# Kernel optimization log

Hardware: AMD Instinct MI355X
Metric: run time of the kernel (lower is better)

The kernel has to match this reference:

```python
import jax, jax.numpy as jnp
import numpy as np
from functools import partial

K = 3
P = K * K * K          # 27 kernel points
G = 2                  # groups
PAD = 1
STRIDE = 1
DIL = 1
AXIS_SCALE = (0.5, 1.0, 1.0)   # (x, y, z) offset axis scale
CUR_SCALE = 0.5                # warmup scale at global_step=0
EPS = 1e-5


def setup_inputs() -> dict:
    key = jax.random.key(0)
    ks = jax.random.split(key, 8)
    C, OC = 64, 64
    N, D, H, W = 1, 32, 32, 32
    inp = {
        "x": jax.random.normal(ks[0], (N, C, D, H, W), jnp.float32),
        "dw_w": jax.random.normal(ks[1], (C, 1, K, K, K), jnp.float32) * 0.1,
        "gn_w": jnp.ones((C,), jnp.float32),
        "gn_b": jnp.zeros((C,), jnp.float32),
        "inp_w": jax.random.normal(ks[2], (C, C), jnp.float32) * (1.0 / np.sqrt(C)),
        "inp_b": jnp.zeros((C,), jnp.float32),
        # offset/mask weights are zero-init in the module; use small random values
        # so the deformable sampling path is exercised nontrivially.
        "off_w": jax.random.normal(ks[3], (C, G * P * 3), jnp.float32) * 0.01,
        "off_b": jnp.zeros((G * P * 3,), jnp.float32),
        "mask_w": jax.random.normal(ks[4], (C, G * P), jnp.float32) * 0.01,
        "mask_b": jnp.tile(jnp.full((P,), -5.0, jnp.float32).at[P // 2].set(0.0), (G,)),
        "out_w": jax.random.normal(ks[5], (C, OC), jnp.float32) * (1.0 / np.sqrt(C)),
        "out_b": jnp.zeros((OC,), jnp.float32),
    }
    return inp


def _trilinear(vol, loc):
    # vol: [Dp, Hp, Wp, gc]; loc: [..., 3] with (x, y, z) in [-1, 1]
    # grid_sample semantics: align_corners=False, padding_mode='zeros'
    Dp, Hp, Wp, _ = vol.shape
    ix = (loc[..., 0] + 1.0) * 0.5 * Wp - 0.5
    iy = (loc[..., 1] + 1.0) * 0.5 * Hp - 0.5
    iz = (loc[..., 2] + 1.0) * 0.5 * Dp - 0.5
    x0f, y0f, z0f = jnp.floor(ix), jnp.floor(iy), jnp.floor(iz)
    fx, fy, fz = ix - x0f, iy - y0f, iz - z0f
    x0, y0, z0 = x0f.astype(jnp.int32), y0f.astype(jnp.int32), z0f.astype(jnp.int32)
    out = jnp.zeros(loc.shape[:-1] + (vol.shape[-1],), vol.dtype)
    for dz in (0, 1):
        wz = fz if dz else 1.0 - fz
        cz = z0 + dz
        for dy in (0, 1):
            wy = fy if dy else 1.0 - fy
            cy = y0 + dy
            for dx in (0, 1):
                wx = fx if dx else 1.0 - fx
                cx = x0 + dx
                valid = ((cz >= 0) & (cz < Dp) & (cy >= 0) & (cy < Hp)
                         & (cx >= 0) & (cx < Wp))
                v = vol[jnp.clip(cz, 0, Dp - 1),
                        jnp.clip(cy, 0, Hp - 1),
                        jnp.clip(cx, 0, Wp - 1)]  # [..., gc]
                out = out + (wz * wy * wx * valid.astype(vol.dtype))[..., None] * v
    return out


def _forward(x, dw_w, gn_w, gn_b, inp_w, inp_b, off_w, off_b,
             mask_w, mask_b, out_w, out_b):
    N, C, D, H, W = x.shape
    gc = C // G
    # --- dw_conv: depthwise conv3d + GroupNorm(1, C) + GELU ---
    xc = jax.lax.conv_general_dilated(
        x, dw_w, window_strides=(1, 1, 1), padding=[(PAD, PAD)] * 3,
        dimension_numbers=("NCDHW", "OIDHW", "NCDHW"), feature_group_count=C)
    mu = xc.mean(axis=(1, 2, 3, 4), keepdims=True)
    var = ((xc - mu) ** 2).mean(axis=(1, 2, 3, 4), keepdims=True)
    xn = (xc - mu) * jax.lax.rsqrt(var + EPS)
    xn = xn * gn_w[None, :, None, None, None] + gn_b[None, :, None, None, None]
    x1 = jnp.transpose(jax.nn.gelu(xn), (0, 2, 3, 4, 1))       # [N,D,H,W,C]
    # --- offset / mask / input projection ---
    offset = x1 @ off_w + off_b                                  # [N,D,H,W,G*P*3]
    mask = jax.nn.softmax(
        (x1 @ mask_w + mask_b).reshape(N, D, H, W, G, P), axis=-1)
    xp = jnp.transpose(x, (0, 2, 3, 4, 1)) @ inp_w + inp_b       # [N,D,H,W,C]
    # --- core deformable sampling ---
    x_pad = jnp.pad(xp, ((0, 0), (PAD, PAD), (PAD, PAD), (PAD, PAD), (0, 0)))
    Dp, Hp, Wp = D + 2 * PAD, H + 2 * PAD, W + 2 * PAD
    Do = (D + 2 * PAD - DIL * (K - 1) - 1) // STRIDE + 1
    Ho = (H + 2 * PAD - DIL * (K - 1) - 1) // STRIDE + 1
    Wo = (W + 2 * PAD - DIL * (K - 1) - 1) // STRIDE + 1
    # reference grid (x/Wp, y/Hp, z/Dp)
    zc, yc, xc_ = jnp.meshgrid(jnp.arange(Do, dtype=jnp.float32),
                               jnp.arange(Ho, dtype=jnp.float32),
                               jnp.arange(Wo, dtype=jnp.float32), indexing="ij")
    ref = jnp.stack(((xc_ * STRIDE + PAD + 0.5) / Wp,
                     (yc * STRIDE + PAD + 0.5) / Hp,
                     (zc * STRIDE + PAD + 0.5) / Dp), axis=-1)   # [Do,Ho,Wo,3]
    # kernel grid
    lin = jnp.linspace(-(K - 1) // 2, (K - 1) // 2, K, dtype=jnp.float32)
    kz, ky, kx = jnp.meshgrid(lin, lin, lin, indexing="ij")
    kgrid = jnp.stack((kx * DIL / Wp, ky * DIL / Hp, kz * DIL / Dp),
                      axis=-1).reshape(P, 3)
    off = offset.reshape(N, Do, Ho, Wo, G, P, 3)
    off_norm = off / jnp.array([Wp, Hp, Dp], jnp.float32)
    axis = jnp.array(AXIS_SCALE, jnp.float32)
    loc = (ref[None, :, :, :, None, None, :]
           + kgrid[None, None, None, None, None, :, :]
           + off_norm * axis * CUR_SCALE)
    loc = loc * 2.0 - 1.0                                        # [N,Do,Ho,Wo,G,P,3]
    vol = jnp.transpose(x_pad.reshape(N, Dp, Hp, Wp, G, gc),
                        (0, 4, 1, 2, 3, 5))                      # [N,G,Dp,Hp,Wp,gc]
    locs = jnp.transpose(loc, (0, 4, 1, 2, 3, 5, 6))             # [N,G,Do,Ho,Wo,P,3]
    sampled = jax.vmap(jax.vmap(_trilinear))(vol, locs)          # [N,G,Do,Ho,Wo,P,gc]
    out = jnp.einsum("ngdhwpc,ndhwgp->ndhwgc", sampled, mask)
    out = out.reshape(N, Do, Ho, Wo, C)
    return out @ out_w + out_b                                   # [N,Do,Ho,Wo,OC]


def reference(x, dw_w, gn_w, gn_b, inp_w, inp_b, off_w, off_b,
              mask_w, mask_b, out_w, out_b):
    return _forward(x, dw_w, gn_w, gn_b, inp_w, inp_b, off_w, off_b,
                    mask_w, mask_b, out_w, out_b)
```

## Files before the change

kernel.cpp:

```cpp
#include <hip/hip_runtime.h>
#include <hip/hip_fp16.h>
#include <math.h>

#define SP 32768
#define PW 38
#define PW2 (PW*PW)
#define PVOX (PW*PW*PW)
#define OMS 228

typedef short bf16x8 __attribute__((ext_vector_type(8)));
typedef unsigned short u16x4 __attribute__((ext_vector_type(4)));
typedef float f32x4 __attribute__((ext_vector_type(4)));

__device__ __forceinline__ unsigned short f2b(float f) {
    unsigned u = __float_as_uint(f);
    u = (u + 0x7FFFu + ((u >> 16) & 1u)) >> 16;
    return (unsigned short)u;
}
__device__ __forceinline__ float b2f1(unsigned short s) {
    return __uint_as_float(((unsigned)s) << 16);
}
__device__ __forceinline__ __half2 h2(unsigned u) {
    return *reinterpret_cast<__half2*>(&u);
}
__device__ __forceinline__ int vox_of(int sb, int v) {
    int tw = sb & 7, th = (sb >> 3) & 15, td = sb >> 7;
    int vw = v & 3, vh = (v >> 2) & 1, vd = v >> 3;
    return (((td << 1) + vd) << 10) + (((th << 1) + vh) << 5) + (tw << 2) + vw;
}

__global__ void k_front(const float* __restrict__ x, const float* __restrict__ dw,
                        const float* __restrict__ off_w, const float* __restrict__ mask_w,
                        const float* __restrict__ off_b, const float* __restrict__ mask_b,
                        const float* __restrict__ inp_w, const float* __restrict__ out_w,
                        unsigned short* __restrict__ WcatB, float* __restrict__ bcat,
                        unsigned short* __restrict__ inpB, unsigned short* __restrict__ outB,
                        unsigned short* __restrict__ x_tb,
                        unsigned short* __restrict__ xcb, float* __restrict__ partials,
                        unsigned short* __restrict__ xpad) {
    int bb = blockIdx.x, tid = threadIdx.x;
    if (bb < 88) {
        int idx = bb * 256 + tid;
        int j = idx >> 6, k = idx & 63;
        if (j < 224) {
            float v = 0.f;
            if (j < 162) v = off_w[k * 162 + j];
            else if (j < 216) v = mask_w[k * 54 + (j - 162)];
            WcatB[j * 64 + k] = f2b(v);
            if (k == 0) bcat[j] = (j < 162) ? off_b[j] : (j < 216 ? mask_b[j - 162] : 0.f);
        } else if (j < 288) {
            outB[(j - 224) * 64 + k] = f2b(out_w[k * 64 + (j - 224)]);
        } else {
            inpB[(j - 288) * 64 + k] = f2b(inp_w[k * 64 + (j - 288)]);
        }
        return;
    }
    if (bb < 600) {
        __shared__ unsigned short tile[64][66];
        int s0 = (bb - 88) * 64;
        int row = tid >> 6, lane = tid & 63;
        for (int c = row; c < 64; c += 4)
            tile[c][lane] = f2b(x[(size_t)c * SP + s0 + lane]);
        __syncthreads();
        for (int r = row; r < 64; r += 4)
            x_tb[(size_t)(s0 + r) * 64 + lane] = tile[lane][r];
        return;
    }
    if (bb < 2648) {
        int b4 = bb - 600;
        int e4 = b4 * 256 + tid;
        int c = e4 >> 13, s4 = (e4 & 8191) << 2;
        int d = s4 >> 10, h = (s4 >> 5) & 31, w0 = s4 & 31;
        const float* xs = x + (size_t)c * SP;
        const float* wt = dw + c * 27;
        float a0 = 0.f, a1 = 0.f, a2 = 0.f, a3 = 0.f;
#pragma unroll
        for (int kd = 0; kd < 3; ++kd) {
            int zz = d + kd - 1; if ((unsigned)zz >= 32u) continue;
#pragma unroll
            for (int kh = 0; kh < 3; ++kh) {
                int yy = h + kh - 1; if ((unsigned)yy >= 32u) continue;
                const float* row = xs + (zz << 10) + (yy << 5) + w0;
                float4 L = *(const float4*)row;
                float xl = (w0 > 0) ? row[-1] : 0.f;
                float xr = (w0 < 28) ? row[4] : 0.f;
                const float* wr = wt + kd * 9 + kh * 3;
                float wm = wr[0], wc = wr[1], wp = wr[2];
                a0 = __builtin_fmaf(wm, xl,  __builtin_fmaf(wc, L.x, __builtin_fmaf(wp, L.y, a0)));
                a1 = __builtin_fmaf(wm, L.x, __builtin_fmaf(wc, L.y, __builtin_fmaf(wp, L.z, a1)));
                a2 = __builtin_fmaf(wm, L.y, __builtin_fmaf(wc, L.z, __builtin_fmaf(wp, L.w, a2)));
                a3 = __builtin_fmaf(wm, L.z, __builtin_fmaf(wc, L.w, __builtin_fmaf(wp, xr,  a3)));
            }
        }
        u16x4 o4; o4[0] = f2b(a0); o4[1] = f2b(a1); o4[2] = f2b(a2); o4[3] = f2b(a3);
        *(u16x4*)(xcb + (size_t)e4 * 4) = o4;
        __shared__ float rs[256], rq[256];
        rs[tid] = a0 + a1 + a2 + a3;
        rq[tid] = a0 * a0 + a1 * a1 + a2 * a2 + a3 * a3;
        __syncthreads();
        for (int off = 128; off > 0; off >>= 1) {
            if (tid < off) { rs[tid] += rs[tid + off]; rq[tid] += rq[tid + off]; }
            __syncthreads();
        }
        if (tid == 0) {
            partials[b4 * 2 + 0] = rs[0];
            partials[b4 * 2 + 1] = rq[0];
        }
        return;
    }
    int cblk = bb - 2648;
    int j = tid >> 4, c4 = tid & 15;
    u16x4 z = {0, 0, 0, 0};
#pragma unroll
    for (int k = 0; k < 4; ++k) {
        int v = cblk * 64 + k * 16 + j;
        if (v >= PVOX) break;
        int zz = v / PW2, r = v - zz * PW2, yy = r / PW, xx = r - yy * PW;
        if (zz < 2 || zz > 33 || yy < 2 || yy > 33 || xx < 2 || xx > 33)
            *(u16x4*)(xpad + (size_t)v * 64 + c4 * 4) = z;
    }
}

__global__ void k_mid(const unsigned short* __restrict__ xcb, const float* __restrict__ partials,
                      const float* __restrict__ gn_w, const float* __restrict__ gn_b,
                      unsigned short* __restrict__ x1b,
                      const unsigned short* __restrict__ x_tb,
                      const unsigned short* __restrict__ inpB,
                      const float* __restrict__ inp_b,
                      unsigned short* __restrict__ xpad) {
    int bb = blockIdx.x, tid = threadIdx.x;
    if (bb < 512) {
        __shared__ float rs[256], rq[256];
        __shared__ unsigned short tile[64][66];
        float a = 0.f, b = 0.f;
        for (int i = tid; i < 2048; i += 256) { a += partials[2 * i]; b += partials[2 * i + 1]; }
        rs[tid] = a; rq[tid] = b;
        __syncthreads();
        for (int off = 128; off > 0; off >>= 1) {
            if (tid < off) { rs[tid] += rs[tid + off]; rq[tid] += rq[tid + off]; }
            __syncthreads();
        }
        const float Minv = 1.f / 2097152.f;
        float mu = rs[0] * Minv;
        float var = rq[0] * Minv - mu * mu;
        float rsq = rsqrtf(var + 1e-5f);
        int s0 = bb * 64;
        int row = tid >> 6, lane = tid & 63;
        for (int c = row; c < 64; c += 4) {
            float v = (b2f1(xcb[(size_t)c * SP + s0 + lane]) - mu) * rsq * gn_w[c] + gn_b[c];
            float t2 = 1.5957691216057308f * (v + 0.044715f * v * v * v);
            tile[c][lane] = f2b(v / (1.f + __expf(-t2)));
        }
        __syncthreads();
        for (int r = row; r < 64; r += 4)
            x1b[(size_t)(s0 + r) * 64 + lane] = tile[lane][r];
        return;
    }
    {
        int wv = tid >> 6, lane = tid & 63;
        int quad = lane >> 4, col = lane & 15;
        int s0 = (bb - 512) * 64 + wv * 16;
        bf16x8 a0 = *(const bf16x8*)(x_tb + (size_t)(s0 + col) * 64 + quad * 8);
        bf16x8 a1 = *(const bf16x8*)(x_tb + (size_t)(s0 + col) * 64 + 32 + quad * 8);
        int vp[4];
#pragma unroll
        for (int r = 0; r < 4; ++r) {
            int s = s0 + (quad << 2) + r;
            vp[r] = (((s >> 10) + 2) * PW + ((s >> 5) & 31) + 2) * PW + (s & 31) + 2;
        }
#pragma unroll
        for (int nt = 0; nt < 4; ++nt) {
            int n0 = nt * 16;
            bf16x8 b0 = *(const bf16x8*)(inpB + (n0 + col) * 64 + quad * 8);
            bf16x8 b1 = *(const bf16x8*)(inpB + (n0 + col) * 64 + 32 + quad * 8);
            f32x4 c = {0.f, 0.f, 0.f, 0.f};
            c = __builtin_amdgcn_mfma_f32_16x16x32_bf16(a0, b0, c, 0, 0, 0);
            c = __builtin_amdgcn_mfma_f32_16x16x32_bf16(a1, b1, c, 0, 0, 0);
            float bq = inp_b[n0 + col];
#pragma unroll
            for (int r = 0; r < 4; ++r)
                xpad[(size_t)vp[r] * 64 + n0 + col] =
                    __half_as_ushort(__float2half(c[r] + bq));
        }
    }
}

template<int P0, int NP>
__device__ __forceinline__ void sampleN(const float* __restrict__ orow,
                                        const float* __restrict__ mrow,
                                        const char* __restrict__ volc,
                                        float xb, float yb, float zb,
                                        float* __restrict__ acc) {
#pragma unroll
    for (int i = 0; i < NP; ++i) {
        const int p = P0 + i;
        const int px = p % 3, py = (p / 3) % 3, pz = p / 9;
        float ox = orow[p * 3 + 0], oy = orow[p * 3 + 1], oz = orow[p * 3 + 2];
        float mk = mrow[p];
        float ix = __builtin_fmaf(0.25f, ox, xb + (float)px);
        float iy = __builtin_fmaf(0.5f, oy, yb + (float)py);
        float iz = __builtin_fmaf(0.5f, oz, zb + (float)pz);
        ix = fminf(fmaxf(ix, 0.f), 36.f);
        iy = fminf(fmaxf(iy, 0.f), 36.f);
        iz = fminf(fmaxf(iz, 0.f), 36.f);
        float xf = floorf(ix), yf = floorf(iy), zf = floorf(iz);
        float fx = ix - xf, fy = iy - yf, fz = iz - zf;
        float fi = __builtin_fmaf(zf, (float)PW2, __builtin_fmaf(yf, (float)PW, xf));
        int ib = ((int)fi) << 7;
        const char* base = volc + ib;
        uint4 r000 = *(const uint4*)(base);
        uint4 r001 = *(const uint4*)(base + 128);
        uint4 r010 = *(const uint4*)(base + PW * 128);
        uint4 r011 = *(const uint4*)(base + PW * 128 + 128);
        uint4 r100 = *(const uint4*)(base + PW2 * 128);
        uint4 r101 = *(const uint4*)(base + PW2 * 128 + 128);
        uint4 r110 = *(const uint4*)(base + (PW2 + PW) * 128);
        uint4 r111 = *(const uint4*)(base + (PW2 + PW) * 128 + 128);
        __half2 fx2 = __float2half2_rn(fx);
        __half2 fy2 = __float2half2_rn(fy);
        __half2 fz2 = __float2half2_rn(fz);
        #define TRI(comp, ci)                                                   \
        {                                                                       \
            __half2 t0 = __hfma2(fx2, __hsub2(h2(r001.comp), h2(r000.comp)), h2(r000.comp)); \
            __half2 t1 = __hfma2(fx2, __hsub2(h2(r011.comp), h2(r010.comp)), h2(r010.comp)); \
            __half2 t2 = __hfma2(fx2, __hsub2(h2(r101.comp), h2(r100.comp)), h2(r100.comp)); \
            __half2 t3 = __hfma2(fx2, __hsub2(h2(r111.comp), h2(r110.comp)), h2(r110.comp)); \
            __half2 u0 = __hfma2(fy2, __hsub2(t1, t0), t0);                     \
            __half2 u1 = __hfma2(fy2, __hsub2(t3, t2), t2);                     \
            __half2 rr = __hfma2(fz2, __hsub2(u1, u0), u0);                     \
            float2 ff = __half22float2(rr);                                     \
            acc[2 * ci + 0] = __builtin_fmaf(mk, ff.x, acc[2 * ci + 0]);        \
            acc[2 * ci + 1] = __builtin_fmaf(mk, ff.y, acc[2 * ci + 1]);        \
        }
        TRI(x, 0) TRI(y, 1) TRI(z, 2) TRI(w, 3)
        #undef TRI
    }
}

template<int P0, int NP>
__device__ __forceinline__ void sampleL(const float* __restrict__ orow,
                                        const float* __restrict__ mrow,
                                        const char* __restrict__ volp,
                                        float xb, float yb, float zb,
                                        float* __restrict__ acc) {
    float ox[NP], oy[NP], oz[NP], mk[NP];
#pragma unroll
    for (int i = 0; i < NP; ++i) {
        ox[i] = orow[(P0 + i) * 3 + 0];
        oy[i] = orow[(P0 + i) * 3 + 1];
        oz[i] = orow[(P0 + i) * 3 + 2];
        mk[i] = mrow[P0 + i];
    }
#pragma unroll
    for (int i = 0; i < NP; ++i) {
        const int p = P0 + i;
        const int px = p % 3, py = (p / 3) % 3, pz = p / 9;
        float ix = __builtin_fmaf(0.25f, ox[i], xb + (float)px);
        float iy = __builtin_fmaf(0.5f, oy[i], yb + (float)py);
        float iz = __builtin_fmaf(0.5f, oz[i], zb + (float)pz);
        ix = fminf(fmaxf(ix, 0.f), 6.999f);
        iy = fminf(fmaxf(iy, 0.f), 4.999f);
        iz = fminf(fmaxf(iz, 0.f), 4.999f);
        float xf = floorf(ix), yf = floorf(iy), zf = floorf(iz);
        float fx = ix - xf, fy = iy - yf, fz = iz - zf;
        float fi = __builtin_fmaf(zf, 48.f, __builtin_fmaf(yf, 8.f, xf));
        int rr = (int)fi;
        #define RD(o) (*(const uint4*)(volp + ((rr + (o)) << 7)))
        uint4 r000 = RD(0);
        uint4 r001 = RD(1);
        uint4 r010 = RD(8);
        uint4 r011 = RD(9);
        uint4 r100 = RD(48);
        uint4 r101 = RD(49);
        uint4 r110 = RD(56);
        uint4 r111 = RD(57);
        #undef RD
        __half2 fx2 = __float2half2_rn(fx);
        __half2 fy2 = __float2half2_rn(fy);
        __half2 fz2 = __float2half2_rn(fz);
        float m = mk[i];
        #define TRI(comp, ci)                                                   \
        {                                                                       \
            __half2 t0 = __hfma2(fx2, __hsub2(h2(r001.comp), h2(r000.comp)), h2(r000.comp)); \
            __half2 t1 = __hfma2(fx2, __hsub2(h2(r011.comp), h2(r010.comp)), h2(r010.comp)); \
            __half2 t2 = __hfma2(fx2, __hsub2(h2(r101.comp), h2(r100.comp)), h2(r100.comp)); \
            __half2 t3 = __hfma2(fx2, __hsub2(h2(r111.comp), h2(r110.comp)), h2(r110.comp)); \
            __half2 u0 = __hfma2(fy2, __hsub2(t1, t0), t0);                     \
            __half2 u1 = __hfma2(fy2, __hsub2(t3, t2), t2);                     \
            __half2 rr2 = __hfma2(fz2, __hsub2(u1, u0), u0);                    \
            float2 ff = __half22float2(rr2);                                    \
            acc[2 * ci + 0] = __builtin_fmaf(m, ff.x, acc[2 * ci + 0]);         \
            acc[2 * ci + 1] = __builtin_fmaf(m, ff.y, acc[2 * ci + 1]);         \
        }
        TRI(x, 0) TRI(y, 1) TRI(z, 2) TRI(w, 3)
        #undef TRI
    }
}

__global__ void __launch_bounds__(256, 2) k_main(const unsigned short* __restrict__ x1b,
                                                 const unsigned short* __restrict__ xpad,
                                                 const unsigned short* __restrict__ WcatB,
                                                 const float* __restrict__ bcat,
                                                 const unsigned short* __restrict__ outB,
                                                 const float* __restrict__ out_b,
                                                 float* __restrict__ out) {
    __shared__ float om_s[16 * OMS];
    __shared__ unsigned short smb[16 * 72];
    __shared__ char vol[288 * 128];
    __shared__ float pbuf[16 * 64];
    int tid = threadIdx.x, wv = tid >> 6, lane = tid & 63;
    int quad = lane >> 4, col = lane & 15;
    int sb = ((blockIdx.x & 7) << 8) | (blockIdx.x >> 3);
    int tw = sb & 7, th = (sb >> 3) & 15, td = sb >> 7;
    {
        const char* xp = (const char*)xpad;
#pragma unroll
        for (int k = 0; k < 3; ++k) {
            uint4 t[3];
#pragma unroll
            for (int j = 0; j < 3; ++j) {
                int u = tid + (k * 3 + j) * 256;
                int rr = u >> 3, ch = u & 7;
                int dz = rr / 48, rem = rr - dz * 48, dy = rem >> 3, dx = rem & 7;
                int pv = ((2 * td + dz) * PW + (2 * th + dy)) * PW + 4 * tw + dx;
                t[j] = *(const uint4*)(xp + ((size_t)pv << 7) + (ch << 4));
            }
#pragma unroll
            for (int j = 0; j < 3; ++j) {
                int u = tid + (k * 3 + j) * 256;
                *(uint4*)(vol + (u << 4)) = t[j];
            }
        }
    }
    {
        int sv = vox_of(sb, col);
        bf16x8 a0 = *(const bf16x8*)(x1b + (size_t)sv * 64 + quad * 8);
        bf16x8 a1 = *(const bf16x8*)(x1b + (size_t)sv * 64 + 32 + quad * 8);
        for (int jt = wv; jt < 14; jt += 4) {
            int n0 = jt * 16;
            bf16x8 b0 = *(const bf16x8*)(WcatB + (n0 + col) * 64 + quad * 8);
            bf16x8 b1 = *(const bf16x8*)(WcatB + (n0 + col) * 64 + 32 + quad * 8);
            f32x4 c = {0.f, 0.f, 0.f, 0.f};
            c = __builtin_amdgcn_mfma_f32_16x16x32_bf16(a0, b0, c, 0, 0, 0);
            c = __builtin_amdgcn_mfma_f32_16x16x32_bf16(a1, b1, c, 0, 0, 0);
            float bb = bcat[n0 + col];
            int n = n0 + col, slot;
            if (n < 162) slot = n + ((n >= 81) ? 3 : 0);
            else { int n2 = n - 162; slot = 168 + n2 + ((n2 >= 27) ? 1 : 0); }
            if (n < 216) {
#pragma unroll
                for (int r = 0; r < 4; ++r)
                    om_s[(quad * 4 + r) * OMS + slot] = c[r] + bb;
            }
        }
    }
    __syncthreads();
    {
        int row = lane >> 2, sub = lane & 3;
        int vloc = (wv & 1) * 8 + (row >> 1), g = row & 1;
        float* m = &om_s[vloc * OMS + 168 + g * 28];
        float mv[7];
        float mx = -1e30f;
#pragma unroll
        for (int i = 0; i < 7; ++i) {
            int p = sub * 7 + i;
            mv[i] = (p < 27) ? m[p] : -1e30f;
            mx = fmaxf(mx, mv[i]);
        }
        mx = fmaxf(mx, __shfl_xor(mx, 1));
        mx = fmaxf(mx, __shfl_xor(mx, 2));
        float e[7], sm = 0.f;
#pragma unroll
        for (int i = 0; i < 7; ++i) { e[i] = __expf(mv[i] - mx); sm += e[i]; }
        sm += __shfl_xor(sm, 1);
        sm += __shfl_xor(sm, 2);
        float inv = 1.f / sm;
#pragma unroll
        for (int i = 0; i < 7; ++i) {
            int p = sub * 7 + i;
            if (p < 27) m[p] = e[i] * inv;
        }
    }
    {
        int half = wv & 1, mode = wv >> 1;
        int v = half * 8 + (lane >> 3);
        int oct = lane & 7, gg = oct >> 2;
        const float* orow = &om_s[v * OMS + gg * 84];
        const float* mrow = &om_s[v * OMS + 168 + gg * 28];
        float acc[8] = {0.f, 0.f, 0.f, 0.f, 0.f, 0.f, 0.f, 0.f};
        if (mode == 0) {
            int sv = vox_of(sb, v);
            float zb = (float)((sv >> 10) + 1);
            float yb = (float)(((sv >> 5) & 31) + 1);
            float xb = (float)((sv & 31) + 1);
            sampleN<0, 9>(orow, mrow, (const char*)xpad + oct * 16, xb, yb, zb, acc);
        } else {
            int vw = v & 3, vh = (v >> 2) & 1, vd = v >> 3;
            sampleL<9, 18>(orow, mrow, vol + oct * 16,
                           (float)(vw + 1), (float)(vh + 1), (float)(vd + 1), acc);
            float* pp = &pbuf[v * 64 + oct * 8];
            *(f32x4*)(pp) = *(f32x4*)(acc);
            *(f32x4*)(pp + 4) = *(f32x4*)(acc + 4);
        }
        __syncthreads();
        if (mode == 0) {
            const float* pp = &pbuf[v * 64 + oct * 8];
            bf16x8 sb8;
#pragma unroll
            for (int k = 0; k < 8; ++k) sb8[k] = (short)f2b(acc[k] + pp[k]);
            *(bf16x8*)(smb + v * 72 + oct * 8) = sb8;
        }
    }
    __syncthreads();
    {
        bf16x8 oa0 = *(const bf16x8*)(smb + col * 72 + quad * 8);
        bf16x8 oa1 = *(const bf16x8*)(smb + col * 72 + 32 + quad * 8);
        int n0 = wv * 16;
        bf16x8 b0 = *(const bf16x8*)(outB + (n0 + col) * 64 + quad * 8);
        bf16x8 b1 = *(const bf16x8*)(outB + (n0 + col) * 64 + 32 + quad * 8);
        f32x4 c = {0.f, 0.f, 0.f, 0.f};
        c = __builtin_amdgcn_mfma_f32_16x16x32_bf16(oa0, b0, c, 0, 0, 0);
        c = __builtin_amdgcn_mfma_f32_16x16x32_bf16(oa1, b1, c, 0, 0, 0);
        float bb = out_b[n0 + col];
        int vr[4];
#pragma unroll
        for (int r = 0; r < 4; ++r) vr[r] = vox_of(sb, quad * 4 + r);
#pragma unroll
        for (int r = 0; r < 4; ++r)
            out[(size_t)vr[r] * 64 + n0 + col] = c[r] + bb;
    }
}

extern "C" void kernel_launch(void* const* d_in, const int* in_sizes, int n_in,
                              void* d_out, int out_size, void* d_ws, size_t ws_size,
                              hipStream_t stream) {
    const float* x      = (const float*)d_in[0];
    const float* dw_w   = (const float*)d_in[1];
    const float* gn_w   = (const float*)d_in[2];
    const float* gn_b   = (const float*)d_in[3];
    const float* inp_w  = (const float*)d_in[4];
    const float* inp_b  = (const float*)d_in[5];
    const float* off_w  = (const float*)d_in[6];
    const float* off_b  = (const float*)d_in[7];
    const float* mask_w = (const float*)d_in[8];
    const float* mask_b = (const float*)d_in[9];
    const float* out_w  = (const float*)d_in[10];
    const float* out_b  = (const float*)d_in[11];

    char* B = (char*)d_ws;
    float*          partials = (float*)(B + 256);
    unsigned short* xcb      = (unsigned short*)(B + 65792);
    unsigned short* x1b      = (unsigned short*)(B + 8454400);
    unsigned short* x_tb     = (unsigned short*)(B + 12648704);
    unsigned short* xpad     = (unsigned short*)(B + 16843008);
    unsigned short* WcatB    = (unsigned short*)(B + 30890240);
    float*          bcat     = (float*)(B + 30918912);
    unsigned short* inpB     = (unsigned short*)(B + 30919936);
    unsigned short* outB     = (unsigned short*)(B + 30928128);
    float* out = (float*)d_out;

    k_front<<<88 + 512 + 2048 + 858, 256, 0, stream>>>(x, dw_w, off_w, mask_w, off_b, mask_b,
                                                       inp_w, out_w, WcatB, bcat, inpB, outB,
                                                       x_tb, xcb, partials, xpad);
    k_mid<<<512 + 512, 256, 0, stream>>>(xcb, partials, gn_w, gn_b, x1b,
                                         x_tb, inpB, inp_b, xpad);
    k_main<<<2048, 256, 0, stream>>>(x1b, xpad, WcatB, bcat, outB, out_b, out);
}
```

Before: 152.8 us.

## Fuse x transpose into input-projection blocks and use wave-shuffle reductions

```diff
diff --git a/kernel.cpp b/kernel.cpp
--- a/kernel.cpp
+++ b/kernel.cpp
@@ -35,7 +35,6 @@
                         const float* __restrict__ inp_w, const float* __restrict__ out_w,
                         unsigned short* __restrict__ WcatB, float* __restrict__ bcat,
                         unsigned short* __restrict__ inpB, unsigned short* __restrict__ outB,
-                        unsigned short* __restrict__ x_tb,
                         unsigned short* __restrict__ xcb, float* __restrict__ partials,
                         unsigned short* __restrict__ xpad) {
     int bb = blockIdx.x, tid = threadIdx.x;
@@ -55,19 +54,8 @@
         }
         return;
     }
-    if (bb < 600) {
-        __shared__ unsigned short tile[64][66];
-        int s0 = (bb - 88) * 64;
-        int row = tid >> 6, lane = tid & 63;
-        for (int c = row; c < 64; c += 4)
-            tile[c][lane] = f2b(x[(size_t)c * SP + s0 + lane]);
-        __syncthreads();
-        for (int r = row; r < 64; r += 4)
-            x_tb[(size_t)(s0 + r) * 64 + lane] = tile[lane][r];
-        return;
-    }
-    if (bb < 2648) {
-        int b4 = bb - 600;
+    if (bb < 2136) {
+        int b4 = bb - 88;
         int e4 = b4 * 256 + tid;
         int c = e4 >> 13, s4 = (e4 & 8191) << 2;
         int d = s4 >> 10, h = (s4 >> 5) & 31, w0 = s4 & 31;
@@ -94,21 +82,24 @@
         }
         u16x4 o4; o4[0] = f2b(a0); o4[1] = f2b(a1); o4[2] = f2b(a2); o4[3] = f2b(a3);
         *(u16x4*)(xcb + (size_t)e4 * 4) = o4;
-        __shared__ float rs[256], rq[256];
-        rs[tid] = a0 + a1 + a2 + a3;
-        rq[tid] = a0 * a0 + a1 * a1 + a2 * a2 + a3 * a3;
+        float s1 = a0 + a1 + a2 + a3;
+        float s2 = a0 * a0 + a1 * a1 + a2 * a2 + a3 * a3;
+#pragma unroll
+        for (int off = 32; off > 0; off >>= 1) {
+            s1 += __shfl_xor(s1, off);
+            s2 += __shfl_xor(s2, off);
+        }
+        __shared__ float ws[8];
+        int wv = tid >> 6, lane = tid & 63;
+        if (lane == 0) { ws[wv * 2] = s1; ws[wv * 2 + 1] = s2; }
         __syncthreads();
-        for (int off = 128; off > 0; off >>= 1) {
-            if (tid < off) { rs[tid] += rs[tid + off]; rq[tid] += rq[tid + off]; }
-            __syncthreads();
-        }
         if (tid == 0) {
-            partials[b4 * 2 + 0] = rs[0];
-            partials[b4 * 2 + 1] = rq[0];
+            partials[b4 * 2 + 0] = ws[0] + ws[2] + ws[4] + ws[6];
+            partials[b4 * 2 + 1] = ws[1] + ws[3] + ws[5] + ws[7];
         }
         return;
     }
-    int cblk = bb - 2648;
+    int cblk = bb - 2136;
     int j = tid >> 4, c4 = tid & 15;
     u16x4 z = {0, 0, 0, 0};
 #pragma unroll
@@ -124,7 +115,7 @@
 __global__ void k_mid(const unsigned short* __restrict__ xcb, const float* __restrict__ partials,
                       const float* __restrict__ gn_w, const float* __restrict__ gn_b,
                       unsigned short* __restrict__ x1b,
-                      const unsigned short* __restrict__ x_tb,
+                      const float* __restrict__ x,
                       const unsigned short* __restrict__ inpB,
                       const float* __restrict__ inp_b,
                       unsigned short* __restrict__ xpad) {
@@ -157,11 +148,16 @@
         return;
     }
     {
-        int wv = tid >> 6, lane = tid & 63;
-        int quad = lane >> 4, col = lane & 15;
-        int s0 = (bb - 512) * 64 + wv * 16;
-        bf16x8 a0 = *(const bf16x8*)(x_tb + (size_t)(s0 + col) * 64 + quad * 8);
-        bf16x8 a1 = *(const bf16x8*)(x_tb + (size_t)(s0 + col) * 64 + 32 + quad * 8);
+        __shared__ unsigned short tileT[64][72];
+        int s0b = (bb - 512) * 64;
+        int row = tid >> 6, lane = tid & 63;
+        for (int c = row; c < 64; c += 4)
+            tileT[lane][c] = f2b(x[(size_t)c * SP + s0b + lane]);
+        __syncthreads();
+        int wv = row, quad = lane >> 4, col = lane & 15;
+        int s0 = s0b + wv * 16;
+        bf16x8 a0 = *(const bf16x8*)(&tileT[wv * 16 + col][quad * 8]);
+        bf16x8 a1 = *(const bf16x8*)(&tileT[wv * 16 + col][32 + quad * 8]);
         int vp[4];
 #pragma unroll
         for (int r = 0; r < 4; ++r) {
@@ -451,7 +447,6 @@
     float*          partials = (float*)(B + 256);
     unsigned short* xcb      = (unsigned short*)(B + 65792);
     unsigned short* x1b      = (unsigned short*)(B + 8454400);
-    unsigned short* x_tb     = (unsigned short*)(B + 12648704);
     unsigned short* xpad     = (unsigned short*)(B + 16843008);
     unsigned short* WcatB    = (unsigned short*)(B + 30890240);
     float*          bcat     = (float*)(B + 30918912);
@@ -459,10 +454,10 @@
     unsigned short* outB     = (unsigned short*)(B + 30928128);
     float* out = (float*)d_out;
 
-    k_front<<<88 + 512 + 2048 + 858, 256, 0, stream>>>(x, dw_w, off_w, mask_w, off_b, mask_b,
-                                                       inp_w, out_w, WcatB, bcat, inpB, outB,
-                                                       x_tb, xcb, partials, xpad);
+    k_front<<<88 + 2048 + 858, 256, 0, stream>>>(x, dw_w, off_w, mask_w, off_b, mask_b,
+                                                 inp_w, out_w, WcatB, bcat, inpB, outB,
+                                                 xcb, partials, xpad);
     k_mid<<<512 + 512, 256, 0, stream>>>(xcb, partials, gn_w, gn_b, x1b,
-                                         x_tb, inpB, inp_b, xpad);
+                                         x, inpB, inp_b, xpad);
     k_main<<<2048, 256, 0, stream>>>(x1b, xpad, WcatB, bcat, outB, out_b, out);
 }
```

Measured after the change: 149.8 us. 1.02x faster.
